# Kernel tuning notes

Hardware: AMD Instinct MI355X
Metric: run time of the kernel (lower is better)

Reference implementation:

```python
import jax, jax.numpy as jnp
import numpy as np

WS = 11      # window_size
SIGMA = 1.5
C1 = 0.01 ** 2
C2 = 0.03 ** 2


def _window(channel):
    g = np.exp(-((np.arange(WS) - WS // 2) ** 2) / (2.0 * SIGMA ** 2))
    g = (g / g.sum()).astype(np.float32)
    w2 = np.outer(g, g)  # [WS, WS]
    return jnp.asarray(np.broadcast_to(w2, (channel, 1, WS, WS)).copy())


def _blur(x, w, channel):
    pad = WS // 2
    return jax.lax.conv_general_dilated(
        x, w, window_strides=(1, 1), padding=[(pad, pad), (pad, pad)],
        dimension_numbers=("NCHW", "OIHW", "NCHW"),
        feature_group_count=channel)


def _ssim(img1, img2, w, channel):
    mu1 = _blur(img1, w, channel)
    mu2 = _blur(img2, w, channel)
    mu1_sq = mu1 * mu1
    mu2_sq = mu2 * mu2
    mu1_mu2 = mu1 * mu2
    sigma1_sq = _blur(img1 * img1, w, channel) - mu1_sq
    sigma2_sq = _blur(img2 * img2, w, channel) - mu2_sq
    sigma12 = _blur(img1 * img2, w, channel) - mu1_mu2
    ssim_map = ((2.0 * mu1_mu2 + C1) * (2.0 * sigma12 + C2)) / (
        (mu1_sq + mu2_sq + C1) * (sigma1_sq + sigma2_sq + C2))
    return ssim_map.mean()  # size_average=True


def setup_inputs() -> dict:
    key = jax.random.key(0)
    k1, k2, k3 = jax.random.split(key, 3)
    B, C, H, W = 16, 3, 512, 512
    return {
        "fused_img": jax.random.uniform(k1, (B, C, H, W), dtype=jnp.float32),
        "source_img1": jax.random.uniform(k2, (B, C, H, W), dtype=jnp.float32),
        "source_img2": jax.random.uniform(k3, (B, C, H, W), dtype=jnp.float32),
    }


def reference(fused_img, source_img1, source_img2):
    channel = fused_img.shape[1]
    w = _window(channel).astype(fused_img.dtype)
    ssim1 = _ssim(fused_img, source_img1, w, channel)
    ssim2 = _ssim(fused_img, source_img2, w, channel)
    return 1.0 - (ssim1 + ssim2) / 2.0
```

## Files before the change

### kernel.cpp

```cpp
#include <hip/hip_runtime.h>
#include <hip/hip_fp16.h>
#include <cmath>
#include <cstring>

#define HALO 5
#define TSX 32
#define TILE_H 128
#define NCHUNK 4
#define CH 32
#define RING 42
#define HSTR 36
#define PLANE (RING * HSTR)
#define WIDTH 512
#define HEIGHT 512

struct GW { float g[11]; uint32_t wpk[11]; };

typedef float f32x2 __attribute__((ext_vector_type(2)));

__device__ __forceinline__ uint32_t pk2(float a, float b)
{
    auto h = __builtin_amdgcn_cvt_pkrtz(a, b);
    return __builtin_bit_cast(uint32_t, h);
}

__device__ __forceinline__ float ssim2(float mu1, float mu2,
                                       float x2b, float y2b, float xyb)
{
    const float C1 = 1e-4f, C2 = 9e-4f;
    float mu12 = mu1 * mu2;
    float num  = (2.f * mu12 + C1) * (2.f * (xyb - mu12) + C2);
    float den  = (mu1 * mu1 + mu2 * mu2 + C1) *
                 ((x2b - mu1 * mu1) + (y2b - mu2 * mu2) + C2);
    return num * __builtin_amdgcn_rcpf(den);
}

template<bool CX, bool CY>
__device__ __forceinline__ void hblur_row(
    const float* __restrict__ rowf, const float* __restrict__ rowa,
    const float* __restrict__ rowb, bool yok, int gx0, int slot, int qA,
    uint32_t (* __restrict__ hb)[PLANE], const GW& gw)
{
    f32x2 acc[4][4];
    #pragma unroll
    for (int jj = 0; jj < 4; ++jj)
        #pragma unroll
        for (int p = 0; p < 4; ++p) acc[jj][p] = f32x2{0.f, 0.f};

    #pragma unroll
    for (int k = 0; k < 5; ++k) {
        const int g = gx0 + 4 * k;
        float4 vf, va, vb;
        if (CX || CY) {
            bool ok = true;
            if (CY) ok = yok;
            if (CX) ok = ok && ((unsigned)g <= (unsigned)(WIDTH - 4));
            vf = ok ? *(const float4*)(rowf + g) : make_float4(0,0,0,0);
            va = ok ? *(const float4*)(rowa + g) : make_float4(0,0,0,0);
            vb = ok ? *(const float4*)(rowb + g) : make_float4(0,0,0,0);
        } else {
            vf = *(const float4*)(rowf + g);
            va = *(const float4*)(rowa + g);
            vb = *(const float4*)(rowb + g);
        }
        const float fs[4] = { vf.x, vf.y, vf.z, vf.w };
        const float as[4] = { va.x, va.y, va.z, va.w };
        const float bs[4] = { vb.x, vb.y, vb.z, vb.w };
        #pragma unroll
        for (int cc = 0; cc < 4; ++cc) {
            const int tt = 4 * k + cc - 3;
            if (tt < 0 || tt > 13) continue;
            const float f = fs[cc], a = as[cc], b = bs[cc];
            f32x2 P[4];
            P[0] = f32x2{f, a};
            P[1] = f32x2{b, f * f};
            P[2] = f32x2{a * a, b * b};
            P[3] = f32x2{f * a, f * b};
            #pragma unroll
            for (int jj = 0; jj < 4; ++jj) {
                const int u = tt - jj;
                if (u >= 0 && u <= 10) {
                    const float w = gw.g[u];
                    const f32x2 w2 = {w, w};
                    #pragma unroll
                    for (int p = 0; p < 4; ++p)
                        acc[jj][p] = __builtin_elementwise_fma(w2, P[p],
                                                               acc[jj][p]);
                }
            }
        }
    }
    #pragma unroll
    for (int p = 0; p < 4; ++p) {
        uint4 v = make_uint4(pk2(acc[0][p].x, acc[0][p].y),
                             pk2(acc[1][p].x, acc[1][p].y),
                             pk2(acc[2][p].x, acc[2][p].y),
                             pk2(acc[3][p].x, acc[3][p].y));
        *(uint4*)(&hb[p][slot * HSTR + 4 * qA]) = v;
    }
}

template<bool CX, bool CY>
__device__ __forceinline__ float tile_compute(
    const float* __restrict__ fI, const float* __restrict__ aI,
    const float* __restrict__ bI, uint32_t (* __restrict__ hb)[PLANE],
    const GW& gw, int tid, int x0, int y0, size_t pbase)
{
    const int rA  = tid >> 3;
    const int qA  = tid & 7;
    const int gx0 = x0 + 4 * qA - 8;
    const int jB  = tid & 31;
    const int rgB = tid >> 5;

    float part = 0.f;

    {
        const int yy = y0 - HALO + rA;
        const bool yok = CY ? ((unsigned)yy < (unsigned)HEIGHT) : true;
        hblur_row<CX, CY>(fI + pbase + (size_t)yy * WIDTH,
                          aI + pbase + (size_t)yy * WIDTH,
                          bI + pbase + (size_t)yy * WIDTH,
                          yok, gx0, rA, qA, hb, gw);
    }
    if (rA < 10) {
        const int t  = 32 + rA;
        const int yy = y0 - HALO + t;
        const bool yok = CY ? ((unsigned)yy < (unsigned)HEIGHT) : true;
        hblur_row<CX, CY>(fI + pbase + (size_t)yy * WIDTH,
                          aI + pbase + (size_t)yy * WIDTH,
                          bI + pbase + (size_t)yy * WIDTH,
                          yok, gx0, t, qA, hb, gw);
    }
    __syncthreads();

    #pragma unroll 1
    for (int c = 0; c < NCHUNK; ++c) {
        if (c) {
            const int t = CH * c + 10 + rA;
            int slot = t;
            slot -= (slot >= RING) ? RING : 0;
            slot -= (slot >= RING) ? RING : 0;
            slot -= (slot >= RING) ? RING : 0;
            const int yy = y0 - HALO + t;
            const bool yok = CY ? ((unsigned)yy < (unsigned)HEIGHT) : true;
            hblur_row<CX, CY>(fI + pbase + (size_t)yy * WIDTH,
                              aI + pbase + (size_t)yy * WIDTH,
                              bI + pbase + (size_t)yy * WIDTH,
                              yok, gx0, slot, qA, hb, gw);
            __syncthreads();
        }

        int sb = CH * c + 4 * rgB;
        sb -= (sb >= RING) ? RING : 0;
        sb -= (sb >= RING) ? RING : 0;
        __half2 acc2[4][4];
        #pragma unroll
        for (int ri = 0; ri < 4; ++ri)
            #pragma unroll
            for (int p = 0; p < 4; ++p)
                acc2[ri][p] = __float2half2_rn(0.f);
        #pragma unroll
        for (int k = 0; k < 14; ++k) {
            int t = sb + k;
            t -= (t >= RING) ? RING : 0;
            const uint32_t* hp = &hb[0][t * HSTR + jB];
            __half2 hv[4];
            #pragma unroll
            for (int p = 0; p < 4; ++p)
                hv[p] = __builtin_bit_cast(__half2, hp[p * PLANE]);
            #pragma unroll
            for (int ri = 0; ri < 4; ++ri) {
                const int u = k - ri;
                if (u >= 0 && u <= 10) {
                    const __half2 w = __builtin_bit_cast(__half2, gw.wpk[u]);
                    #pragma unroll
                    for (int p = 0; p < 4; ++p)
                        acc2[ri][p] = __hfma2(w, hv[p], acc2[ri][p]);
                }
            }
        }
        #pragma unroll
        for (int ri = 0; ri < 4; ++ri) {
            const float F  = __low2float (acc2[ri][0]);
            const float A  = __high2float(acc2[ri][0]);
            const float B  = __low2float (acc2[ri][1]);
            const float F2 = __high2float(acc2[ri][1]);
            const float A2 = __low2float (acc2[ri][2]);
            const float B2 = __high2float(acc2[ri][2]);
            const float FA = __low2float (acc2[ri][3]);
            const float FB = __high2float(acc2[ri][3]);
            part += ssim2(F, A, F2, A2, FA);
            part += ssim2(F, B, F2, B2, FB);
        }
        __syncthreads();
    }
    return part;
}

__global__ __launch_bounds__(256, 3)
void ssim_tile(const float* __restrict__ fI, const float* __restrict__ aI,
               const float* __restrict__ bI, float* __restrict__ bsum,
               GW gw)
{
    __shared__ __align__(16) uint32_t hb[4][PLANE];
    __shared__ float red[4];

    const int tid = threadIdx.x;
    const int x0 = blockIdx.x * TSX;
    const int y0 = blockIdx.y * TILE_H;
    const size_t pbase = (size_t)blockIdx.z * (size_t)(WIDTH * HEIGHT);

    const bool ex = (blockIdx.x == 0) || (blockIdx.x == gridDim.x - 1);
    const bool ey = (blockIdx.y == 0) || (blockIdx.y == gridDim.y - 1);

    float part;
    if (!ex && !ey)
        part = tile_compute<false, false>(fI, aI, bI, hb, gw, tid, x0, y0, pbase);
    else if (!ex)
        part = tile_compute<false, true >(fI, aI, bI, hb, gw, tid, x0, y0, pbase);
    else if (!ey)
        part = tile_compute<true,  false>(fI, aI, bI, hb, gw, tid, x0, y0, pbase);
    else
        part = tile_compute<true,  true >(fI, aI, bI, hb, gw, tid, x0, y0, pbase);

    #pragma unroll
    for (int off = 32; off > 0; off >>= 1) part += __shfl_down(part, off);
    if ((tid & 63) == 0) red[tid >> 6] = part;
    __syncthreads();
    if (tid == 0) {
        int bid = blockIdx.x + gridDim.x * (blockIdx.y + gridDim.y * blockIdx.z);
        bsum[bid] = red[0] + red[1] + red[2] + red[3];
    }
}

__global__ __launch_bounds__(256)
void ssim_final(const float* __restrict__ bsum, float* __restrict__ out,
                int nb, float invTwoN)
{
    __shared__ float sred[4];
    float s = 0.f;
    for (int i = threadIdx.x; i < nb; i += 256) s += bsum[i];
    #pragma unroll
    for (int off = 32; off > 0; off >>= 1) s += __shfl_down(s, off);
    if ((threadIdx.x & 63) == 0) sred[threadIdx.x >> 6] = s;
    __syncthreads();
    if (threadIdx.x == 0)
        out[0] = 1.f - (sred[0] + sred[1] + sred[2] + sred[3]) * invTwoN;
}

static uint16_t f2h(float f)
{
    uint32_t x; std::memcpy(&x, &f, 4);
    uint32_t s = (x >> 16) & 0x8000u;
    int      e = (int)((x >> 23) & 0xff) - 127 + 15;
    uint32_t m = x & 0x007fffffu;
    uint32_t base = ((uint32_t)e << 10) | (m >> 13);
    uint32_t rem  = m & 0x1fffu;
    if (rem > 0x1000u || (rem == 0x1000u && (base & 1u))) base++;
    return (uint16_t)(s | base);
}

extern "C" void kernel_launch(void* const* d_in, const int* in_sizes, int n_in,
                              void* d_out, int out_size, void* d_ws, size_t ws_size,
                              hipStream_t stream)
{
    const float* f  = (const float*)d_in[0];
    const float* s1 = (const float*)d_in[1];
    const float* s2 = (const float*)d_in[2];
    float* out  = (float*)d_out;
    float* bsum = (float*)d_ws;

    const int N = in_sizes[0];
    const int planes = N / (WIDTH * HEIGHT);

    GW gw;
    double gd[11], gs = 0.0;
    for (int i = 0; i < 11; ++i) {
        double d = (double)(i - 5);
        gd[i] = exp(-(d * d) / 4.5);
        gs += gd[i];
    }
    for (int i = 0; i < 11; ++i) {
        gw.g[i] = (float)(gd[i] / gs);
        uint32_t h = f2h(gw.g[i]);
        gw.wpk[i] = (h << 16) | h;
    }

    dim3 grid(WIDTH / TSX, HEIGHT / TILE_H, planes);
    const int nb = (WIDTH / TSX) * (HEIGHT / TILE_H) * planes;
    ssim_tile<<<grid, dim3(256), 0, stream>>>(f, s1, s2, bsum, gw);
    ssim_final<<<1, dim3(256), 0, stream>>>(bsum, out, nb, 0.5f / (float)N);
}
```

Measured before the change: 229.2 us.

## Prefetch next chunk's rows before vertical pass and trim halo loads

Global loads for the next chunk's horizontal-blur rows are now issued before the current chunk's vertical blur and SSIM computation, and consumed afterwards, so load latency overlaps compute. The row fragment loading is also narrowed from five float4 loads to one scalar, three float4 and one scalar, dropping unused halo elements. The cost is higher register pressure from holding three prefetched fragments across the vertical pass, which may hurt occupancy under launch_bounds(256,3).

```diff
diff --git a/kernel.cpp b/kernel.cpp
--- a/kernel.cpp
+++ b/kernel.cpp
@@ -35,12 +35,50 @@
     return num * __builtin_amdgcn_rcpf(den);
 }
 
+struct RowFrag { float s0; float4 q1, q2, q3; float s4; };
+
 template<bool CX, bool CY>
-__device__ __forceinline__ void hblur_row(
-    const float* __restrict__ rowf, const float* __restrict__ rowa,
-    const float* __restrict__ rowb, bool yok, int gx0, int slot, int qA,
-    uint32_t (* __restrict__ hb)[PLANE], const GW& gw)
-{
+__device__ __forceinline__ void load_frag(
+    const float* __restrict__ row, bool yok, int gx0, RowFrag& r)
+{
+    const int g3 = gx0 + 3, gq1 = gx0 + 4, gq2 = gx0 + 8, gq3 = gx0 + 12,
+              g16 = gx0 + 16;
+    if (CX || CY) {
+        bool okS0 = true, okQ1 = true, okQ2 = true, okQ3 = true, okS4 = true;
+        if (CY) { okS0 = okQ1 = okQ2 = okQ3 = okS4 = yok; }
+        if (CX) {
+            okS0 = okS0 && ((unsigned)g3  <  (unsigned)WIDTH);
+            okQ1 = okQ1 && ((unsigned)gq1 <= (unsigned)(WIDTH - 4));
+            okQ2 = okQ2 && ((unsigned)gq2 <= (unsigned)(WIDTH - 4));
+            okQ3 = okQ3 && ((unsigned)gq3 <= (unsigned)(WIDTH - 4));
+            okS4 = okS4 && ((unsigned)g16 <  (unsigned)WIDTH);
+        }
+        r.s0 = okS0 ? row[g3] : 0.f;
+        r.q1 = okQ1 ? *(const float4*)(row + gq1) : make_float4(0,0,0,0);
+        r.q2 = okQ2 ? *(const float4*)(row + gq2) : make_float4(0,0,0,0);
+        r.q3 = okQ3 ? *(const float4*)(row + gq3) : make_float4(0,0,0,0);
+        r.s4 = okS4 ? row[g16] : 0.f;
+    } else {
+        r.s0 = row[g3];
+        r.q1 = *(const float4*)(row + gq1);
+        r.q2 = *(const float4*)(row + gq2);
+        r.q3 = *(const float4*)(row + gq3);
+        r.s4 = row[g16];
+    }
+}
+
+#define UNPACK(r, e) \
+    { e[0]=r.s0; e[1]=r.q1.x; e[2]=r.q1.y; e[3]=r.q1.z; e[4]=r.q1.w; \
+      e[5]=r.q2.x; e[6]=r.q2.y; e[7]=r.q2.z; e[8]=r.q2.w; \
+      e[9]=r.q3.x; e[10]=r.q3.y; e[11]=r.q3.z; e[12]=r.q3.w; e[13]=r.s4; }
+
+__device__ __forceinline__ void hblur_core(
+    const RowFrag& rf, const RowFrag& ra, const RowFrag& rb,
+    int slot, int qA, uint32_t (* __restrict__ hb)[PLANE], const GW& gw)
+{
+    float ef[14], ea[14], eb[14];
+    UNPACK(rf, ef); UNPACK(ra, ea); UNPACK(rb, eb);
+
     f32x2 acc[4][4];
     #pragma unroll
     for (int jj = 0; jj < 4; ++jj)
@@ -48,45 +86,23 @@
         for (int p = 0; p < 4; ++p) acc[jj][p] = f32x2{0.f, 0.f};
 
     #pragma unroll
-    for (int k = 0; k < 5; ++k) {
-        const int g = gx0 + 4 * k;
-        float4 vf, va, vb;
-        if (CX || CY) {
-            bool ok = true;
-            if (CY) ok = yok;
-            if (CX) ok = ok && ((unsigned)g <= (unsigned)(WIDTH - 4));
-            vf = ok ? *(const float4*)(rowf + g) : make_float4(0,0,0,0);
-            va = ok ? *(const float4*)(rowa + g) : make_float4(0,0,0,0);
-            vb = ok ? *(const float4*)(rowb + g) : make_float4(0,0,0,0);
-        } else {
-            vf = *(const float4*)(rowf + g);
-            va = *(const float4*)(rowa + g);
-            vb = *(const float4*)(rowb + g);
-        }
-        const float fs[4] = { vf.x, vf.y, vf.z, vf.w };
-        const float as[4] = { va.x, va.y, va.z, va.w };
-        const float bs[4] = { vb.x, vb.y, vb.z, vb.w };
-        #pragma unroll
-        for (int cc = 0; cc < 4; ++cc) {
-            const int tt = 4 * k + cc - 3;
-            if (tt < 0 || tt > 13) continue;
-            const float f = fs[cc], a = as[cc], b = bs[cc];
-            f32x2 P[4];
-            P[0] = f32x2{f, a};
-            P[1] = f32x2{b, f * f};
-            P[2] = f32x2{a * a, b * b};
-            P[3] = f32x2{f * a, f * b};
-            #pragma unroll
-            for (int jj = 0; jj < 4; ++jj) {
-                const int u = tt - jj;
-                if (u >= 0 && u <= 10) {
-                    const float w = gw.g[u];
-                    const f32x2 w2 = {w, w};
-                    #pragma unroll
-                    for (int p = 0; p < 4; ++p)
-                        acc[jj][p] = __builtin_elementwise_fma(w2, P[p],
-                                                               acc[jj][p]);
-                }
+    for (int tt = 0; tt < 14; ++tt) {
+        const float f = ef[tt], a = ea[tt], b = eb[tt];
+        f32x2 P[4];
+        P[0] = f32x2{f, a};
+        P[1] = f32x2{b, f * f};
+        P[2] = f32x2{a * a, b * b};
+        P[3] = f32x2{f * a, f * b};
+        #pragma unroll
+        for (int jj = 0; jj < 4; ++jj) {
+            const int u = tt - jj;
+            if (u >= 0 && u <= 10) {
+                const float w = gw.g[u];
+                const f32x2 w2 = {w, w};
+                #pragma unroll
+                for (int p = 0; p < 4; ++p)
+                    acc[jj][p] = __builtin_elementwise_fma(w2, P[p],
+                                                           acc[jj][p]);
             }
         }
     }
@@ -117,37 +133,42 @@
     {
         const int yy = y0 - HALO + rA;
         const bool yok = CY ? ((unsigned)yy < (unsigned)HEIGHT) : true;
-        hblur_row<CX, CY>(fI + pbase + (size_t)yy * WIDTH,
-                          aI + pbase + (size_t)yy * WIDTH,
-                          bI + pbase + (size_t)yy * WIDTH,
-                          yok, gx0, rA, qA, hb, gw);
+        const size_t ro = pbase + (size_t)yy * WIDTH;
+        RowFrag rf, ra, rb;
+        load_frag<CX, CY>(fI + ro, yok, gx0, rf);
+        load_frag<CX, CY>(aI + ro, yok, gx0, ra);
+        load_frag<CX, CY>(bI + ro, yok, gx0, rb);
+        hblur_core(rf, ra, rb, rA, qA, hb, gw);
     }
     if (rA < 10) {
         const int t  = 32 + rA;
         const int yy = y0 - HALO + t;
         const bool yok = CY ? ((unsigned)yy < (unsigned)HEIGHT) : true;
-        hblur_row<CX, CY>(fI + pbase + (size_t)yy * WIDTH,
-                          aI + pbase + (size_t)yy * WIDTH,
-                          bI + pbase + (size_t)yy * WIDTH,
-                          yok, gx0, t, qA, hb, gw);
+        const size_t ro = pbase + (size_t)yy * WIDTH;
+        RowFrag rf, ra, rb;
+        load_frag<CX, CY>(fI + ro, yok, gx0, rf);
+        load_frag<CX, CY>(aI + ro, yok, gx0, ra);
+        load_frag<CX, CY>(bI + ro, yok, gx0, rb);
+        hblur_core(rf, ra, rb, t, qA, hb, gw);
     }
     __syncthreads();
 
     #pragma unroll 1
     for (int c = 0; c < NCHUNK; ++c) {
-        if (c) {
-            const int t = CH * c + 10 + rA;
-            int slot = t;
-            slot -= (slot >= RING) ? RING : 0;
-            slot -= (slot >= RING) ? RING : 0;
-            slot -= (slot >= RING) ? RING : 0;
+        RowFrag pf, pa, pb;
+        int slot_n = 0;
+        if (c < NCHUNK - 1) {
+            const int t = CH * (c + 1) + 10 + rA;
+            slot_n = t;
+            slot_n -= (slot_n >= RING) ? RING : 0;
+            slot_n -= (slot_n >= RING) ? RING : 0;
+            slot_n -= (slot_n >= RING) ? RING : 0;
             const int yy = y0 - HALO + t;
-            const bool yok = CY ? ((unsigned)yy < (unsigned)HEIGHT) : true;
-            hblur_row<CX, CY>(fI + pbase + (size_t)yy * WIDTH,
-                              aI + pbase + (size_t)yy * WIDTH,
-                              bI + pbase + (size_t)yy * WIDTH,
-                              yok, gx0, slot, qA, hb, gw);
-            __syncthreads();
+            const bool yokn = CY ? ((unsigned)yy < (unsigned)HEIGHT) : true;
+            const size_t ro = pbase + (size_t)yy * WIDTH;
+            load_frag<CX, CY>(fI + ro, yokn, gx0, pf);
+            load_frag<CX, CY>(aI + ro, yokn, gx0, pa);
+            load_frag<CX, CY>(bI + ro, yokn, gx0, pb);
         }
 
         int sb = CH * c + 4 * rgB;
@@ -193,6 +214,11 @@
             part += ssim2(F, B, F2, B2, FB);
         }
         __syncthreads();
+
+        if (c < NCHUNK - 1) {
+            hblur_core(pf, pa, pb, slot_n, qA, hb, gw);
+            __syncthreads();
+        }
     }
     return part;
 }
```

Result: slower. 430.2 us (+87.7%).
